# Kernel tuning notes

Measured on AMD Instinct MI355X. Metric: run time of the kernel, lower is better.

Reference implementation:

```python
import jax, jax.numpy as jnp
import numpy as np
import math

HIDDEN = 1024
HEADS = 16
HEAD_DIM = HIDDEN // HEADS


def setup_inputs() -> dict:
    key = jax.random.key(0)
    ks = jax.random.split(key, 9)
    B, T, C = 4, 2048, HIDDEN
    s = 0.02
    x = jax.random.normal(ks[0], (B, T, C), dtype=jnp.float32)
    # torch nn.Linear weights are [out_features, in_features]
    Wq = jax.random.normal(ks[1], (C, C), dtype=jnp.float32) * s
    Wk = jax.random.normal(ks[2], (C, C), dtype=jnp.float32) * s
    Wv = jax.random.normal(ks[3], (C, C), dtype=jnp.float32) * s
    Wo = jax.random.normal(ks[4], (C, C), dtype=jnp.float32) * s
    bq = jax.random.normal(ks[5], (C,), dtype=jnp.float32) * s
    bk = jax.random.normal(ks[6], (C,), dtype=jnp.float32) * s
    bv = jax.random.normal(ks[7], (C,), dtype=jnp.float32) * s
    bo = jax.random.normal(ks[8], (C,), dtype=jnp.float32) * s
    return {"x": x, "Wq": Wq, "bq": bq, "Wk": Wk, "bk": bk,
            "Wv": Wv, "bv": bv, "Wo": Wo, "bo": bo}


def reference(x, Wq, bq, Wk, bk, Wv, bv, Wo, bo):
    B, T, C = x.shape
    H, D = HEADS, HEAD_DIM
    # projections: torch Linear => x @ W.T + b
    q = (x @ Wq.T + bq).reshape(B, T, H, D).transpose(0, 2, 1, 3)  # [B,H,T,D]
    k = (x @ Wk.T + bk).reshape(B, T, H, D).transpose(0, 2, 1, 3)
    v = (x @ Wv.T + bv).reshape(B, T, H, D).transpose(0, 2, 1, 3)
    scale = 1.0 / math.sqrt(D)
    scores = jnp.einsum('bhqd,bhkd->bhqk', q, k) * scale  # [B,H,T,T]
    attn = jax.nn.softmax(scores, axis=-1)
    y = jnp.einsum('bhqk,bhkd->bhqd', attn, v)  # [B,H,T,D]
    y = y.transpose(0, 2, 1, 3).reshape(B, T, C)
    return y @ Wo.T + bo
```

## Files before the change

kernel.cpp:

```cpp
#include <hip/hip_runtime.h>
#include <stdint.h>


using u16 = unsigned short;
using u32 = unsigned int;
typedef __attribute__((ext_vector_type(8))) __bf16 bf16x8;
typedef __attribute__((ext_vector_type(4))) float  floatx4;

#define QSCALE 0.18033688011112043f

__device__ __forceinline__ u16 f2b(float f) {
    union { float f; u32 i; } x; x.f = f;
    return (u16)((x.i + 0x7fffu + ((x.i >> 16) & 1u)) >> 16);
}
__device__ __forceinline__ u32 fbits(float f) { union { float f; u32 i; } x; x.f = f; return x.i; }
__device__ __forceinline__ u32 pkbf(float a, float b) {
    u32 ia = fbits(a) + 0x8000u, ib = fbits(b) + 0x8000u;
    return __builtin_amdgcn_perm(ib, ia, 0x07060302u);
}
__device__ __forceinline__ bf16x8 ld16B(const u16* p) {
    bf16x8 v; __builtin_memcpy(&v, p, 16); return v;
}
__device__ __forceinline__ void async16(const u16* g, u16* l) {
    __builtin_amdgcn_global_load_lds((const __attribute__((address_space(1))) unsigned int*)g,
                                     (__attribute__((address_space(3))) unsigned int*)l,
                                     16, 0, 0);
}

__global__ __launch_bounds__(256) void convert_kernel(
    const float* __restrict__ x,
    const float* __restrict__ Wq, const float* __restrict__ Wk,
    const float* __restrict__ Wv, const float* __restrict__ Wo,
    u16* __restrict__ xb, u16* __restrict__ wqb, u16* __restrict__ wkb,
    u16* __restrict__ wvb, u16* __restrict__ wob)
{
    size_t e = ((size_t)blockIdx.x * 256 + threadIdx.x) * 4;
    const float* src; u16* dst; size_t off;
    const size_t XN = (size_t)8 << 20;
    if (e < XN) { src = x; dst = xb; off = e; }
    else {
        size_t k = e - XN;
        int w = (int)(k >> 20);
        off = k & ((1u << 20) - 1);
        src = (w == 0) ? Wq : (w == 1) ? Wk : (w == 2) ? Wv : Wo;
        dst = (w == 0) ? wqb : (w == 1) ? wkb : (w == 2) ? wvb : wob;
    }
    float4 f = *(const float4*)(src + off);
    u32 dws[2] = { pkbf(f.x, f.y), pkbf(f.z, f.w) };
    __builtin_memcpy(dst + off, dws, 8);
}

__device__ __forceinline__ void gemm_loop(const u16* __restrict__ A, const u16* __restrict__ W,
                                          int m0, int n0, floatx4 (&acc)[4][4],
                                          u16* __restrict__ sA, u16* __restrict__ sB)
{
    constexpr int K = 1024;
    const int tid  = threadIdx.x;
    const int wave = tid >> 6, lane = tid & 63;
    const int wr = wave >> 1, wc = wave & 1;
    const int quad = lane >> 4, l15 = lane & 15;

    #pragma unroll
    for (int i = 0; i < 4; ++i)
        #pragma unroll
        for (int j = 0; j < 4; ++j)
            acc[i][j] = (floatx4){0.f, 0.f, 0.f, 0.f};

    #pragma unroll 1
    for (int kb = 0; kb < 16; ++kb) {
        __syncthreads();
        const int k0 = kb * 64;
        #pragma unroll
        for (int j = 0; j < 4; ++j) {
            int r  = wave * 32 + j * 8 + (lane >> 3);
            int kg = (lane & 7) ^ (r & 7);
            async16(A + (size_t)(m0 + r) * K + k0 + kg * 8, &sA[(wave * 32 + j * 8) * 64]);
            async16(W + (size_t)(n0 + r) * K + k0 + kg * 8, &sB[(wave * 32 + j * 8) * 64]);
        }
        __syncthreads();

        #pragma unroll
        for (int kk = 0; kk < 2; ++kk) {
            bf16x8 af[4], bf[4];
            const int kg = kk * 4 + quad;
            #pragma unroll
            for (int t = 0; t < 4; ++t) {
                int ra = wr * 64 + t * 16 + l15;
                af[t] = ld16B(&sA[ra * 64 + ((kg ^ (ra & 7)) * 8)]);
                int rb = wc * 64 + t * 16 + l15;
                bf[t] = ld16B(&sB[rb * 64 + ((kg ^ (rb & 7)) * 8)]);
            }
            #pragma unroll
            for (int mt = 0; mt < 4; ++mt)
                #pragma unroll
                for (int nt = 0; nt < 4; ++nt)
                    acc[mt][nt] = __builtin_amdgcn_mfma_f32_16x16x32_bf16(af[mt], bf[nt], acc[mt][nt], 0, 0, 0);
        }
    }
}

__global__ __launch_bounds__(256) void qkv_kernel(
    const u16* __restrict__ x, const u16* __restrict__ Wcat,
    const float* __restrict__ bq, const float* __restrict__ bk, const float* __restrict__ bv,
    u16* __restrict__ q, u16* __restrict__ k, u16* __restrict__ vt)
{
    __shared__ __align__(16) u16 sA[128 * 64];
    __shared__ __align__(16) u16 sB[128 * 64];
    const int m0 = blockIdx.y * 128, n0 = blockIdx.x * 128;
    floatx4 acc[4][4];
    gemm_loop(x, Wcat, m0, n0, acc, sA, sB);

    const int tid = threadIdx.x;
    const int wave = tid >> 6, lane = tid & 63;
    const int wr = wave >> 1, wc = wave & 1;
    const int quad = lane >> 4, l15 = lane & 15;

    const int z = n0 >> 10;
    const float* bb = (z == 0) ? bq : (z == 1) ? bk : bv;
    const float scale = (z == 0) ? QSCALE : 1.0f;
    u16* o = (z == 0) ? q : k;

    #pragma unroll
    for (int nt = 0; nt < 4; ++nt) {
        int col  = n0 + wc * 64 + nt * 16 + l15;
        int c    = col & 1023;
        float bv_ = bb[c];
        #pragma unroll
        for (int mt = 0; mt < 4; ++mt) {
            int row0 = m0 + wr * 64 + mt * 16 + quad * 4;
            if (z == 2) {
                float v0 = acc[mt][nt][0] + bv_, v1 = acc[mt][nt][1] + bv_;
                float v2 = acc[mt][nt][2] + bv_, v3 = acc[mt][nt][3] + bv_;
                u32 dws[2] = { pkbf(v0, v1), pkbf(v2, v3) };
                int b = row0 >> 11, t0 = row0 & 2047;
                size_t idx = ((size_t)((b * 16 + (c >> 6)) * 64 + (c & 63)) * 2048) + t0;
                __builtin_memcpy(vt + idx, dws, 8);
            } else {
                #pragma unroll
                for (int r = 0; r < 4; ++r) {
                    float v = (acc[mt][nt][r] + bv_) * scale;
                    o[(size_t)(row0 + r) * 1024 + c] = f2b(v);
                }
            }
        }
    }
}

__global__ __launch_bounds__(256) void proj_kernel(
    const u16* __restrict__ y, const u16* __restrict__ Wo, const float* __restrict__ bo,
    float* __restrict__ out)
{
    __shared__ __align__(16) u16 sA[128 * 64];
    __shared__ __align__(16) u16 sB[128 * 64];
    const int m0 = blockIdx.y * 128, n0 = blockIdx.x * 128;
    floatx4 acc[4][4];
    gemm_loop(y, Wo, m0, n0, acc, sA, sB);

    const int tid = threadIdx.x;
    const int wave = tid >> 6, lane = tid & 63;
    const int wr = wave >> 1, wc = wave & 1;
    const int quad = lane >> 4, l15 = lane & 15;

    #pragma unroll
    for (int nt = 0; nt < 4; ++nt) {
        int col = n0 + wc * 64 + nt * 16 + l15;
        float bv_ = bo[col];
        #pragma unroll
        for (int mt = 0; mt < 4; ++mt) {
            int row0 = m0 + wr * 64 + mt * 16 + quad * 4;
            #pragma unroll
            for (int r = 0; r < 4; ++r)
                out[(size_t)(row0 + r) * 1024 + col] = acc[mt][nt][r] + bv_;
        }
    }
}

__global__ __launch_bounds__(256, 2) void attn_kernel(
    const u16* __restrict__ Q, const u16* __restrict__ K,
    const u16* __restrict__ Vt, u16* __restrict__ Y)
{
    const int bh = blockIdx.x, qt = blockIdx.y;
    const int tid = threadIdx.x;
    const int wave = tid >> 6, lane = tid & 63;
    const int quad = lane >> 4, l15 = lane & 15, l7 = l15 & 7;
    const int b = bh >> 4, h = bh & 15;

    __shared__ __align__(16) u16 sK[2][64 * 64];
    __shared__ __align__(16) u16 sV[2][64 * 64];
    __shared__ __align__(16) u16 sP[4][64 * 72];

    const __bf16 one = (__bf16)1.0f;
    const bf16x8 ones = { one, one, one, one, one, one, one, one };

    bf16x8 qf[4][2];
    #pragma unroll
    for (int nt = 0; nt < 4; ++nt) {
        const u16* qp = Q + (size_t)(b * 2048 + qt * 256 + wave * 64 + nt * 16 + l15) * 1024 + h * 64 + quad * 8;
        qf[nt][0] = ld16B(qp);
        qf[nt][1] = ld16B(qp + 32);
    }

    const int r8 = lane >> 3;
    const int g7 = (lane & 7) ^ r8;
    const u16* ksrc = K  + (size_t)(b * 2048 + wave * 16 + r8) * 1024 + h * 64 + g7 * 8;
    const u16* vsrc = Vt + ((size_t)(bh * 64 + wave * 16 + r8)) * 2048 + g7 * 8;

    floatx4 accO[4][4];
    #pragma unroll
    for (int mt = 0; mt < 4; ++mt)
        #pragma unroll
        for (int nt = 0; nt < 4; ++nt) accO[mt][nt] = (floatx4){0.f, 0.f, 0.f, 0.f};
    floatx4 accR[4];
    #pragma unroll
    for (int nt = 0; nt < 4; ++nt) accR[nt] = (floatx4){0.f, 0.f, 0.f, 0.f};

    {
        u16* dK = &sK[0][wave * 16 * 64];
        u16* dV = &sV[0][wave * 16 * 64];
        async16(ksrc,            dK);
        async16(ksrc + 8 * 1024, dK + 8 * 64);
        async16(vsrc,            dV);
        async16(vsrc + 8 * 2048, dV + 8 * 64);
    }
    __syncthreads();

    u16* sp = sP[wave];
    const int spRow = l15 * 72;

    #pragma unroll 1
    for (int kt = 0; kt < 32; ++kt) {
        const int cur = kt & 1;
        if (kt < 31) {
            u16* dK = &sK[cur ^ 1][wave * 16 * 64];
            u16* dV = &sV[cur ^ 1][wave * 16 * 64];
            const u16* ks = ksrc + (size_t)(kt + 1) * 64 * 1024;
            const u16* vs = vsrc + (size_t)(kt + 1) * 64;
            async16(ks,            dK);
            async16(ks + 8 * 1024, dK + 8 * 64);
            async16(vs,            dV);
            async16(vs + 8 * 2048, dV + 8 * 64);
        }
        const u16* bK = sK[cur];
        const u16* bV = sV[cur];

        bf16x8 kf[4][2], vf[4][2];
        #pragma unroll
        for (int mt = 0; mt < 4; ++mt)
            #pragma unroll
            for (int kk = 0; kk < 2; ++kk) {
                kf[mt][kk] = ld16B(&bK[(mt * 16 + l15) * 64 + (((kk * 4 + quad) ^ l7) * 8)]);
                vf[mt][kk] = ld16B(&bV[(mt * 16 + l15) * 64 + (((kk * 4 + quad) ^ l7) * 8)]);
            }

        #pragma unroll
        for (int nt = 0; nt < 4; ++nt) {
            floatx4 st[4];
            #pragma unroll
            for (int mt = 0; mt < 4; ++mt) st[mt] = (floatx4){0.f, 0.f, 0.f, 0.f};
            #pragma unroll
            for (int kk = 0; kk < 2; ++kk)
                #pragma unroll
                for (int mt = 0; mt < 4; ++mt)
                    st[mt] = __builtin_amdgcn_mfma_f32_16x16x32_bf16(kf[mt][kk], qf[nt][kk], st[mt], 0, 0, 0);

            u16* spn = sp + nt * 16 * 72 + spRow;
            #pragma unroll
            for (int mt = 0; mt < 4; ++mt) {
                float p0 = __builtin_amdgcn_exp2f(st[mt][0]);
                float p1 = __builtin_amdgcn_exp2f(st[mt][1]);
                float p2 = __builtin_amdgcn_exp2f(st[mt][2]);
                float p3 = __builtin_amdgcn_exp2f(st[mt][3]);
                u32 dws[2] = { pkbf(p0, p1), pkbf(p2, p3) };
                __builtin_memcpy(spn + mt * 16 + quad * 4, dws, 8);
            }
            bf16x8 pf0 = ld16B(spn + quad * 8);
            bf16x8 pf1 = ld16B(spn + 32 + quad * 8);
            accR[nt] = __builtin_amdgcn_mfma_f32_16x16x32_bf16(ones, pf0, accR[nt], 0, 0, 0);
            accR[nt] = __builtin_amdgcn_mfma_f32_16x16x32_bf16(ones, pf1, accR[nt], 0, 0, 0);
            #pragma unroll
            for (int mt = 0; mt < 4; ++mt) {
                accO[mt][nt] = __builtin_amdgcn_mfma_f32_16x16x32_bf16(vf[mt][0], pf0, accO[mt][nt], 0, 0, 0);
                accO[mt][nt] = __builtin_amdgcn_mfma_f32_16x16x32_bf16(vf[mt][1], pf1, accO[mt][nt], 0, 0, 0);
            }
        }
        __syncthreads();
    }

    float inv[4];
    #pragma unroll
    for (int nt = 0; nt < 4; ++nt) inv[nt] = 1.f / accR[nt][0];
    #pragma unroll
    for (int nt = 0; nt < 4; ++nt)
        #pragma unroll
        for (int mt = 0; mt < 4; ++mt) {
            u32 dws[2] = { pkbf(accO[mt][nt][0] * inv[nt], accO[mt][nt][1] * inv[nt]),
                           pkbf(accO[mt][nt][2] * inv[nt], accO[mt][nt][3] * inv[nt]) };
            __builtin_memcpy(&sp[(nt * 16 + l15) * 72 + mt * 16 + quad * 4], dws, 8);
        }
    const int rl = lane >> 3, cl = lane & 7;
    #pragma unroll
    for (int pass = 0; pass < 8; ++pass) {
        int qq = pass * 8 + rl;
        int t = qt * 256 + wave * 64 + qq;
        bf16x8 vrow = ld16B(&sp[qq * 72 + cl * 8]);
        __builtin_memcpy(Y + ((size_t)(b * 2048 + t)) * 1024 + h * 64 + cl * 8, &vrow, 16);
    }
}

extern "C" void kernel_launch(void* const* d_in, const int* in_sizes, int n_in,
                              void* d_out, int out_size, void* d_ws, size_t ws_size,
                              hipStream_t stream)
{
    const float* x  = (const float*)d_in[0];
    const float* Wq = (const float*)d_in[1];
    const float* bq = (const float*)d_in[2];
    const float* Wk = (const float*)d_in[3];
    const float* bk = (const float*)d_in[4];
    const float* Wv = (const float*)d_in[5];
    const float* bv = (const float*)d_in[6];
    const float* Wo = (const float*)d_in[7];
    const float* bo = (const float*)d_in[8];
    float* out = (float*)d_out;

    const size_t NTOK = (size_t)8192 * 1024;
    const size_t WN   = (size_t)1024 * 1024;
    u16* xb  = (u16*)d_ws;
    u16* wqb = xb + NTOK;
    u16* wkb = wqb + WN;
    u16* wvb = wkb + WN;
    u16* wob = wvb + WN;
    u16* q   = wob + WN;
    u16* k   = q + NTOK;
    u16* vt  = k + NTOK;
    u16* y   = vt + NTOK;

    convert_kernel<<<dim3(12288), 256, 0, stream>>>(x, Wq, Wk, Wv, Wo, xb, wqb, wkb, wvb, wob);
    qkv_kernel<<<dim3(24, 64), 256, 0, stream>>>(xb, wqb, bq, bk, bv, q, k, vt);
    attn_kernel<<<dim3(64, 8), 256, 0, stream>>>(q, k, vt, y);
    proj_kernel<<<dim3(8, 64), 256, 0, stream>>>(y, wob, bo, out);
}
```

Baseline: 269.0 us.

## Double-buffer GEMM LDS tiles and load V fragments directly from global in attention

```diff
diff --git a/kernel.cpp b/kernel.cpp
--- a/kernel.cpp
+++ b/kernel.cpp
@@ -66,18 +66,35 @@
         for (int j = 0; j < 4; ++j)
             acc[i][j] = (floatx4){0.f, 0.f, 0.f, 0.f};
 
+    const int rstage = lane >> 3;
+    const int gstage = lane & 7;
+
+    #pragma unroll
+    for (int j = 0; j < 4; ++j) {
+        int r  = wave * 32 + j * 8 + rstage;
+        int kg = gstage ^ (r & 7);
+        async16(A + (size_t)(m0 + r) * K + kg * 8, &sA[(wave * 32 + j * 8) * 64]);
+        async16(W + (size_t)(n0 + r) * K + kg * 8, &sB[(wave * 32 + j * 8) * 64]);
+    }
+    __syncthreads();
+
     #pragma unroll 1
     for (int kb = 0; kb < 16; ++kb) {
-        __syncthreads();
-        const int k0 = kb * 64;
-        #pragma unroll
-        for (int j = 0; j < 4; ++j) {
-            int r  = wave * 32 + j * 8 + (lane >> 3);
-            int kg = (lane & 7) ^ (r & 7);
-            async16(A + (size_t)(m0 + r) * K + k0 + kg * 8, &sA[(wave * 32 + j * 8) * 64]);
-            async16(W + (size_t)(n0 + r) * K + k0 + kg * 8, &sB[(wave * 32 + j * 8) * 64]);
-        }
-        __syncthreads();
+        const int cur = kb & 1;
+        if (kb < 15) {
+            const int k0 = (kb + 1) * 64;
+            u16* dA = sA + (cur ^ 1) * 8192;
+            u16* dB = sB + (cur ^ 1) * 8192;
+            #pragma unroll
+            for (int j = 0; j < 4; ++j) {
+                int r  = wave * 32 + j * 8 + rstage;
+                int kg = gstage ^ (r & 7);
+                async16(A + (size_t)(m0 + r) * K + k0 + kg * 8, &dA[(wave * 32 + j * 8) * 64]);
+                async16(W + (size_t)(n0 + r) * K + k0 + kg * 8, &dB[(wave * 32 + j * 8) * 64]);
+            }
+        }
+        const u16* bA = sA + cur * 8192;
+        const u16* bB = sB + cur * 8192;
 
         #pragma unroll
         for (int kk = 0; kk < 2; ++kk) {
@@ -86,9 +103,9 @@
             #pragma unroll
             for (int t = 0; t < 4; ++t) {
                 int ra = wr * 64 + t * 16 + l15;
-                af[t] = ld16B(&sA[ra * 64 + ((kg ^ (ra & 7)) * 8)]);
+                af[t] = ld16B(&bA[ra * 64 + ((kg ^ (ra & 7)) * 8)]);
                 int rb = wc * 64 + t * 16 + l15;
-                bf[t] = ld16B(&sB[rb * 64 + ((kg ^ (rb & 7)) * 8)]);
+                bf[t] = ld16B(&bB[rb * 64 + ((kg ^ (rb & 7)) * 8)]);
             }
             #pragma unroll
             for (int mt = 0; mt < 4; ++mt)
@@ -96,16 +113,17 @@
                 for (int nt = 0; nt < 4; ++nt)
                     acc[mt][nt] = __builtin_amdgcn_mfma_f32_16x16x32_bf16(af[mt], bf[nt], acc[mt][nt], 0, 0, 0);
         }
-    }
-}
-
-__global__ __launch_bounds__(256) void qkv_kernel(
+        __syncthreads();
+    }
+}
+
+__global__ __launch_bounds__(256, 2) void qkv_kernel(
     const u16* __restrict__ x, const u16* __restrict__ Wcat,
     const float* __restrict__ bq, const float* __restrict__ bk, const float* __restrict__ bv,
     u16* __restrict__ q, u16* __restrict__ k, u16* __restrict__ vt)
 {
-    __shared__ __align__(16) u16 sA[128 * 64];
-    __shared__ __align__(16) u16 sB[128 * 64];
+    __shared__ __align__(16) u16 sA[2 * 128 * 64];
+    __shared__ __align__(16) u16 sB[2 * 128 * 64];
     const int m0 = blockIdx.y * 128, n0 = blockIdx.x * 128;
     floatx4 acc[4][4];
     gemm_loop(x, Wcat, m0, n0, acc, sA, sB);
@@ -146,12 +164,12 @@
     }
 }
 
-__global__ __launch_bounds__(256) void proj_kernel(
+__global__ __launch_bounds__(256, 2) void proj_kernel(
     const u16* __restrict__ y, const u16* __restrict__ Wo, const float* __restrict__ bo,
     float* __restrict__ out)
 {
-    __shared__ __align__(16) u16 sA[128 * 64];
-    __shared__ __align__(16) u16 sB[128 * 64];
+    __shared__ __align__(16) u16 sA[2 * 128 * 64];
+    __shared__ __align__(16) u16 sB[2 * 128 * 64];
     const int m0 = blockIdx.y * 128, n0 = blockIdx.x * 128;
     floatx4 acc[4][4];
     gemm_loop(y, Wo, m0, n0, acc, sA, sB);
@@ -186,7 +204,6 @@
     const int b = bh >> 4, h = bh & 15;
 
     __shared__ __align__(16) u16 sK[2][64 * 64];
-    __shared__ __align__(16) u16 sV[2][64 * 64];
     __shared__ __align__(16) u16 sP[4][64 * 72];
 
     const __bf16 one = (__bf16)1.0f;
@@ -202,8 +219,8 @@
 
     const int r8 = lane >> 3;
     const int g7 = (lane & 7) ^ r8;
-    const u16* ksrc = K  + (size_t)(b * 2048 + wave * 16 + r8) * 1024 + h * 64 + g7 * 8;
-    const u16* vsrc = Vt + ((size_t)(bh * 64 + wave * 16 + r8)) * 2048 + g7 * 8;
+    const u16* ksrc = K + (size_t)(b * 2048 + wave * 16 + r8) * 1024 + h * 64 + g7 * 8;
+    const u16* vbase = Vt + (size_t)(bh * 64) * 2048;
 
     floatx4 accO[4][4];
     #pragma unroll
@@ -216,11 +233,8 @@
 
     {
         u16* dK = &sK[0][wave * 16 * 64];
-        u16* dV = &sV[0][wave * 16 * 64];
         async16(ksrc,            dK);
         async16(ksrc + 8 * 1024, dK + 8 * 64);
-        async16(vsrc,            dV);
-        async16(vsrc + 8 * 2048, dV + 8 * 64);
     }
     __syncthreads();
 
@@ -232,25 +246,24 @@
         const int cur = kt & 1;
         if (kt < 31) {
             u16* dK = &sK[cur ^ 1][wave * 16 * 64];
-            u16* dV = &sV[cur ^ 1][wave * 16 * 64];
             const u16* ks = ksrc + (size_t)(kt + 1) * 64 * 1024;
-            const u16* vs = vsrc + (size_t)(kt + 1) * 64;
             async16(ks,            dK);
             async16(ks + 8 * 1024, dK + 8 * 64);
-            async16(vs,            dV);
-            async16(vs + 8 * 2048, dV + 8 * 64);
-        }
+        }
+        bf16x8 vf[4][2];
+        #pragma unroll
+        for (int mt = 0; mt < 4; ++mt)
+            #pragma unroll
+            for (int kk = 0; kk < 2; ++kk)
+                vf[mt][kk] = ld16B(vbase + (size_t)(mt * 16 + l15) * 2048 + kt * 64 + (kk * 4 + quad) * 8);
+
         const u16* bK = sK[cur];
-        const u16* bV = sV[cur];
-
-        bf16x8 kf[4][2], vf[4][2];
+        bf16x8 kf[4][2];
         #pragma unroll
         for (int mt = 0; mt < 4; ++mt)
             #pragma unroll
-            for (int kk = 0; kk < 2; ++kk) {
+            for (int kk = 0; kk < 2; ++kk)
                 kf[mt][kk] = ld16B(&bK[(mt * 16 + l15) * 64 + (((kk * 4 + quad) ^ l7) * 8)]);
-                vf[mt][kk] = ld16B(&bV[(mt * 16 + l15) * 64 + (((kk * 4 + quad) ^ l7) * 8)]);
-            }
 
         #pragma unroll
         for (int nt = 0; nt < 4; ++nt) {
```

Result: slower. 274.6 us (+2.1%).
